# Kernel tuning notes

Hardware: AMD Instinct MI355X
Metric: run time of the kernel (lower is better)

## Reference

```python
import jax, jax.numpy as jnp
import numpy as np

N = 8192
F_IN = 256
F_OUT = 128
NEG_BIG = -9.0e15


def setup_inputs() -> dict:
    key = jax.random.key(0)
    k1, k2, k3, k4 = jax.random.split(key, 4)
    x = jax.random.normal(k1, (N, F_IN), dtype=jnp.float32)
    W = jax.random.normal(k2, (F_IN, F_OUT), dtype=jnp.float32) * 0.05
    a = jax.random.normal(k3, (2 * F_OUT, 1), dtype=jnp.float32) * 0.05
    adj = jax.random.randint(k4, (N, N), 0, 2, dtype=jnp.int32)
    return {"x": x, "W": W, "a": a, "adj": adj}


def reference(x, W, a, adj):
    # h = x @ W : [N, F_OUT]
    h = x @ W
    # Original builds [N, N, 2F] concat then matmuls with a. Since
    # a_input[i,j] = concat(h_i, h_j), the score is separable:
    # (a_input @ a)[i,j] = h_i . a[:F] + h_j . a[F:]
    a1 = a[:F_OUT, 0]   # [F_OUT]
    a2 = a[F_OUT:, 0]   # [F_OUT]
    s1 = h @ a1         # [N]
    s2 = h @ a2         # [N]
    e = jax.nn.leaky_relu(s1[:, None] + s2[None, :], negative_slope=0.2)
    e = jnp.where(adj > 0, e, jnp.float32(NEG_BIG))
    attention = jax.nn.softmax(e, axis=1)   # [N, N]
    h_prime = attention @ h                 # [N, F_OUT]
    return jax.nn.elu(h_prime)
```

## Files before the change

kernel.cpp:

```cpp
#include <hip/hip_runtime.h>
#include <math.h>

#define NN 8192

typedef __attribute__((ext_vector_type(8))) short short8;
typedef __attribute__((ext_vector_type(4))) short short4v;
typedef __attribute__((ext_vector_type(4))) float f32x4;
typedef __attribute__((ext_vector_type(4))) int int4v;

#define L2E 1.4426950408889634f

typedef __attribute__((address_space(3))) unsigned lds_u32;
typedef __attribute__((address_space(1))) unsigned g_u32;

__device__ __forceinline__ void gll16(const void* g, void* l) {
    __builtin_amdgcn_global_load_lds((const g_u32*)g, (lds_u32*)l, 16, 0, 0);
}

__device__ __forceinline__ short f2bf(float f) {
    union { float f; unsigned u; } v; v.f = f;
    unsigned r = v.u + 0x7fffu + ((v.u >> 16) & 1u);
    return (short)(r >> 16);
}

__device__ __forceinline__ f32x4 zero4() {
    f32x4 v; v[0] = 0.f; v[1] = 0.f; v[2] = 0.f; v[3] = 0.f; return v;
}

__global__ void k0_wt(const float* __restrict__ W, short* __restrict__ WT) {
    int idx = blockIdx.x * 256 + threadIdx.x;
    if (idx < 256 * 128) {
        int k = idx & 255;
        int f = idx >> 8;
        WT[f * 256 + k] = f2bf(W[k * 128 + f]);
    }
}

__global__ __launch_bounds__(128) void k1_h(
        const float* __restrict__ x, const short* __restrict__ WT,
        const float* __restrict__ a, short* __restrict__ hT,
        float* __restrict__ s1L2E, float* __restrict__ s2L2E) {
    const int w = threadIdx.x >> 6;
    const int l = threadIdx.x & 63;
    const int quad = l >> 4;
    const int fr = l & 15;
    const int i0 = blockIdx.x * 32 + w * 16;

    f32x4 acc[8];
#pragma unroll
    for (int t = 0; t < 8; ++t) acc[t] = zero4();

    const float* xrow = x + (size_t)(i0 + fr) * 256;
#pragma unroll
    for (int kk = 0; kk < 8; ++kk) {
        const int k0 = kk * 32 + quad * 8;
        f32x4 xa = *(const f32x4*)(xrow + k0);
        f32x4 xb = *(const f32x4*)(xrow + k0 + 4);
        short8 av;
#pragma unroll
        for (int e = 0; e < 4; ++e) { av[e] = f2bf(xa[e]); av[4 + e] = f2bf(xb[e]); }
#pragma unroll
        for (int t = 0; t < 8; ++t) {
            short8 bv = *(const short8*)(WT + (t * 16 + fr) * 256 + k0);
            acc[t] = __builtin_amdgcn_mfma_f32_16x16x32_bf16(av, bv, acc[t], 0, 0, 0);
        }
    }

    float s1p[4] = {0.f, 0.f, 0.f, 0.f};
    float s2p[4] = {0.f, 0.f, 0.f, 0.f};
#pragma unroll
    for (int t = 0; t < 8; ++t) {
        float a1v = a[t * 16 + fr];
        float a2v = a[128 + t * 16 + fr];
#pragma unroll
        for (int r = 0; r < 4; ++r) {
            s1p[r] += acc[t][r] * a1v;
            s2p[r] += acc[t][r] * a2v;
        }
    }
#pragma unroll
    for (int r = 0; r < 4; ++r) {
#pragma unroll
        for (int m = 1; m < 16; m <<= 1) {
            s1p[r] += __shfl_xor(s1p[r], m, 64);
            s2p[r] += __shfl_xor(s2p[r], m, 64);
        }
    }
    if (fr == 0) {
#pragma unroll
        for (int r = 0; r < 4; ++r) {
            const int i = i0 + quad * 4 + r;
            s1L2E[i] = s1p[r] * L2E;
            s2L2E[i] = s2p[r] * L2E;
        }
    }

#pragma unroll
    for (int t = 0; t < 8; ++t) {
        short4v hv;
#pragma unroll
        for (int r = 0; r < 4; ++r) hv[r] = f2bf(acc[t][r]);
        *(short4v*)(hT + (size_t)(t * 16 + fr) * NN + i0 + quad * 4) = hv;
    }
}

template<int JSPLIT, bool PARTIAL>
__global__ __launch_bounds__(256, 2) void k2_attn(
        const int* __restrict__ adj, const short* __restrict__ hT,
        const float* __restrict__ s1g, const float* __restrict__ s2g,
        float* __restrict__ pvp, float* __restrict__ zp,
        float* __restrict__ out) {
    constexpr int JW = NN / JSPLIT;
    constexpr int NSTEP = JW / 64;
    constexpr int BUFB = 25600;
    __shared__ __align__(16) char lds_c[3 * BUFB + 256];

    const int tid = threadIdx.x;
    const int w = tid >> 6;
    const int l = tid & 63;
    const int quad = l >> 4;
    const int fr = l & 15;
    const int rh = w >> 1;
    const int wj = w & 1;
    const int rb = blockIdx.x / JSPLIT;
    const int jb = blockIdx.x % JSPLIT;
    const int r32 = rb * 32;
    const int jbb = jb * JW;

    const float S = s1g[r32 + rh * 16 + fr];

    const char* hsrc[4];
    {
        const char* hbase = (const char*)hT;
#pragma unroll
        for (int p = 0; p < 4; ++p) {
            const int o = p * 4096 + tid * 16;
            const int row = o >> 7;
            const int colb = o & 127;
            hsrc[p] = hbase + (size_t)row * (NN * 2) + (size_t)jbb * 2
                    + (colb ^ ((row & 7) << 4));
        }
    }
    const char* asrc[2];
    {
        const char* abase = (const char*)adj;
#pragma unroll
        for (int p = 0; p < 2; ++p) {
            const int o = p * 4096 + tid * 16;
            const int row = o >> 8;
            const int colb = o & 255;
            asrc[p] = abase + (size_t)(r32 + row) * (NN * 4) + (size_t)jbb * 4
                    + (colb ^ ((row & 7) << 4));
        }
    }
    const char* csrc = (const char*)s2g + (size_t)jbb * 4 + (l < 16 ? l * 16 : 240);

    auto STAGE = [&](int jt, int buf) {
        jt = (jt < NSTEP) ? jt : NSTEP - 1;
        char* hd = lds_c + buf * BUFB + w * 1024;
        char* ad = lds_c + buf * BUFB + 16384 + w * 1024;
        char* cd = lds_c + buf * BUFB + 24576;
        const size_t hof = (size_t)jt * 128;
        const size_t aof = (size_t)jt * 256;
#pragma unroll
        for (int p = 0; p < 4; ++p) gll16(hsrc[p] + hof, hd + p * 4096);
#pragma unroll
        for (int p = 0; p < 2; ++p) gll16(asrc[p] + aof, ad + p * 4096);
        gll16(csrc + aof, cd);
    };

    f32x4 acc[8];
#pragma unroll
    for (int t = 0; t < 8; ++t) acc[t] = zero4();
    float zacc = 0.f;

    STAGE(0, 0); STAGE(1, 1); STAGE(2, 2);

    int cur = 0;
    for (int t = 0; t < NSTEP; ++t) {
        asm volatile("s_waitcnt vmcnt(14)" ::: "memory");
        __builtin_amdgcn_s_barrier();
        __builtin_amdgcn_sched_barrier(0);

        const char* hb = lds_c + cur * BUFB;
        const char* ab = lds_c + cur * BUFB + 16384;
        const float* cb = (const float*)(lds_c + cur * BUFB + 24576);

        const int arow = rh * 16 + fr;
        const unsigned aswz = (unsigned)((arow & 7) << 4);
        const unsigned al = (unsigned)(arow * 256 + wj * 128 + quad * 32);
        const int4v g0 = *(const int4v*)(ab + (al ^ aswz));
        const int4v g1 = *(const int4v*)(ab + ((al + 16) ^ aswz));
        const f32x4 c0 = *(const f32x4*)(cb + wj * 32 + quad * 8);
        const f32x4 c1 = *(const f32x4*)(cb + wj * 32 + quad * 8 + 4);

        short8 pa;
        {
            float zs = 0.f;
#pragma unroll
            for (int e = 0; e < 8; ++e) {
                const float cv = (e < 4) ? c0[e & 3] : c1[e & 3];
                const int gv = (e < 4) ? g0[e & 3] : g1[e & 3];
                const float u = S + cv;
                const float tt = fmaxf(u, 0.2f * u);
                const float p = (gv > 0) ? exp2f(tt) : 0.f;
                zs += p;
                pa[e] = f2bf(p);
            }
            zacc += zs;
        }

#pragma unroll
        for (int t8 = 0; t8 < 8; ++t8) {
            const int hrow = t8 * 16 + fr;
            const short8 bv = *(const short8*)(
                hb + ((unsigned)(hrow * 128 + wj * 64 + quad * 16) ^ ((hrow & 7) << 4)));
            acc[t8] = __builtin_amdgcn_mfma_f32_16x16x32_bf16(pa, bv, acc[t8], 0, 0, 0);
        }

        __builtin_amdgcn_sched_barrier(0);
        asm volatile("" ::: "memory");
        __builtin_amdgcn_s_barrier();

        STAGE(t + 3, cur);
        cur = (cur == 2) ? 0 : cur + 1;
    }

    asm volatile("s_waitcnt vmcnt(0)" ::: "memory");
    __syncthreads();

    zacc += __shfl_xor(zacc, 16, 64);
    zacc += __shfl_xor(zacc, 32, 64);
    float* zb = (float*)(lds_c + 3 * BUFB);
    if (l < 16) zb[w * 16 + l] = zacc;

    float* red = (float*)lds_c;
    if (wj == 1) {
#pragma unroll
        for (int t = 0; t < 8; ++t)
            *(f32x4*)(red + rh * 2048 + t * 256 + l * 4) = acc[t];
    }
    __syncthreads();

    if (wj == 0) {
#pragma unroll
        for (int t = 0; t < 8; ++t)
            acc[t] += *(const f32x4*)(red + rh * 2048 + t * 256 + l * 4);
#pragma unroll
        for (int r = 0; r < 4; ++r) {
            const int irow = quad * 4 + r;
            const float z = zb[rh * 32 + irow] + zb[rh * 32 + 16 + irow];
            const int grow = r32 + rh * 16 + irow;
            if (PARTIAL) {
                if (fr == 0) zp[(size_t)jb * NN + grow] = z;
                float* orow = pvp + ((size_t)jb * NN + grow) * 128;
#pragma unroll
                for (int t = 0; t < 8; ++t) orow[t * 16 + fr] = acc[t][r];
            } else {
                const float inv = 1.0f / z;
                float* orow = out + (size_t)grow * 128;
#pragma unroll
                for (int t = 0; t < 8; ++t) {
                    float v = acc[t][r] * inv;
                    orow[t * 16 + fr] = (v > 0.f) ? v : expm1f(v);
                }
            }
        }
    }
}

__global__ __launch_bounds__(256) void k3_fin(
        const float* __restrict__ pvp, const float* __restrict__ zp,
        float* __restrict__ out, int jsplit) {
    const int idx = blockIdx.x * 256 + threadIdx.x;
    const int row = idx >> 5;
    const int c = (idx & 31) << 2;
    f32x4 s = zero4();
    float z = 0.f;
    for (int p = 0; p < jsplit; ++p) {
        s += *(const f32x4*)(pvp + ((size_t)p * NN + row) * 128 + c);
        z += zp[(size_t)p * NN + row];
    }
    const float inv = 1.0f / z;
    f32x4 o;
#pragma unroll
    for (int e = 0; e < 4; ++e) {
        float v = s[e] * inv;
        o[e] = (v > 0.f) ? v : expm1f(v);
    }
    *(f32x4*)(out + (size_t)row * 128 + c) = o;
}

extern "C" void kernel_launch(void* const* d_in, const int* in_sizes, int n_in,
                              void* d_out, int out_size, void* d_ws, size_t ws_size,
                              hipStream_t stream) {
    const float* x   = (const float*)d_in[0];
    const float* W   = (const float*)d_in[1];
    const float* a   = (const float*)d_in[2];
    const int*   adj = (const int*)d_in[3];
    float* out = (float*)d_out;

    char* ws = (char*)d_ws;
    const size_t MB = 1024 * 1024;
    short* hT    = (short*)ws;
    float* s1L2E = (float*)(ws + 2 * MB);
    float* s2L2E = (float*)(ws + 2 * MB + 32768);
    short* WT    = (short*)(ws + 2 * MB + 65536);
    const size_t base = 2 * MB + 131072;

    const size_t need2 = base + 2 * ((size_t)NN * 128 * 4) + 2 * ((size_t)NN * 4);
    const bool js2 = (ws_size >= need2);

    float* pvp = (float*)(ws + base);
    float* zp  = (float*)(ws + base + (size_t)2 * NN * 128 * 4);

    k0_wt<<<128, 256, 0, stream>>>(W, WT);
    k1_h<<<256, 128, 0, stream>>>(x, WT, a, hT, s1L2E, s2L2E);

    if (js2) {
        k2_attn<2, true><<<512, 256, 0, stream>>>(adj, hT, s1L2E, s2L2E, pvp, zp, nullptr);
        k3_fin<<<1024, 256, 0, stream>>>(pvp, zp, out, 2);
    } else {
        k2_attn<1, false><<<256, 256, 0, stream>>>(adj, hT, s1L2E, s2L2E, nullptr, nullptr, out);
    }
}
```

Measured before the change: 94.73 us.

## Replace J-split attention with single-pass kernel using wide adj macro-tiles

Removes the two-way column split and the separate finalize kernel, so each 32-row block now streams all 8192 columns and writes the normalized ELU output directly. Adjacency is staged in 256-column macro tiles of contiguous 1KB row segments, double-buffered, while hT is quad-buffered in 64-column substeps. This is meant to cut partial-sum traffic and the extra launch, and to improve adj load granularity. In exchange it uses about 130KB of LDS, which forces one block per CU and halves resident waves, leaving less latency hiding.

Result: slower. 116.0 us (+22.5%).

```diff
diff --git a/kernel.cpp b/kernel.cpp
--- a/kernel.cpp
+++ b/kernel.cpp
@@ -104,16 +104,13 @@
     }
 }
 
-template<int JSPLIT, bool PARTIAL>
-__global__ __launch_bounds__(256, 2) void k2_attn(
+__global__ __launch_bounds__(256, 1) void k2_attn(
         const int* __restrict__ adj, const short* __restrict__ hT,
         const float* __restrict__ s1g, const float* __restrict__ s2g,
-        float* __restrict__ pvp, float* __restrict__ zp,
         float* __restrict__ out) {
-    constexpr int JW = NN / JSPLIT;
-    constexpr int NSTEP = JW / 64;
-    constexpr int BUFB = 25600;
-    __shared__ __align__(16) char lds_c[3 * BUFB + 256];
+    constexpr int NSUB = NN / 64;
+    constexpr int NMAC = NN / 256;
+    __shared__ __align__(16) char lds_c[133376];
 
     const int tid = threadIdx.x;
     const int w = tid >> 6;
@@ -122,10 +119,7 @@
     const int fr = l & 15;
     const int rh = w >> 1;
     const int wj = w & 1;
-    const int rb = blockIdx.x / JSPLIT;
-    const int jb = blockIdx.x % JSPLIT;
-    const int r32 = rb * 32;
-    const int jbb = jb * JW;
+    const int r32 = blockIdx.x * 32;
 
     const float S = s1g[r32 + rh * 16 + fr];
 
@@ -137,36 +131,32 @@
             const int o = p * 4096 + tid * 16;
             const int row = o >> 7;
             const int colb = o & 127;
-            hsrc[p] = hbase + (size_t)row * (NN * 2) + (size_t)jbb * 2
-                    + (colb ^ ((row & 7) << 4));
-        }
-    }
-    const char* asrc[2];
+            hsrc[p] = hbase + (size_t)row * (NN * 2) + (colb ^ ((row & 7) << 4));
+        }
+    }
+    const char* asrc8[8];
     {
         const char* abase = (const char*)adj;
 #pragma unroll
-        for (int p = 0; p < 2; ++p) {
-            const int o = p * 4096 + tid * 16;
-            const int row = o >> 8;
-            const int colb = o & 255;
-            asrc[p] = abase + (size_t)(r32 + row) * (NN * 4) + (size_t)jbb * 4
-                    + (colb ^ ((row & 7) << 4));
-        }
-    }
-    const char* csrc = (const char*)s2g + (size_t)jbb * 4 + (l < 16 ? l * 16 : 240);
-
-    auto STAGE = [&](int jt, int buf) {
-        jt = (jt < NSTEP) ? jt : NSTEP - 1;
-        char* hd = lds_c + buf * BUFB + w * 1024;
-        char* ad = lds_c + buf * BUFB + 16384 + w * 1024;
-        char* cd = lds_c + buf * BUFB + 24576;
-        const size_t hof = (size_t)jt * 128;
-        const size_t aof = (size_t)jt * 256;
+        for (int p = 0; p < 8; ++p) {
+            const int row = w * 8 + p;
+            asrc8[p] = abase + (size_t)(r32 + row) * (NN * 4) + ((l ^ p) << 4);
+        }
+    }
+    const char* csrc = (const char*)s2g + l * 16;
+
+    auto STAGE_HT = [&](int q, int buf) {
+        char* hd = lds_c + buf * 16384 + w * 1024;
+        const size_t hof = (size_t)q * 128;
 #pragma unroll
         for (int p = 0; p < 4; ++p) gll16(hsrc[p] + hof, hd + p * 4096);
-#pragma unroll
-        for (int p = 0; p < 2; ++p) gll16(asrc[p] + aof, ad + p * 4096);
-        gll16(csrc + aof, cd);
+    };
+    auto STAGE_AC = [&](int m, int buf) {
+        char* ad = lds_c + 65536 + buf * 32768 + w * 8192;
+        const size_t aof = (size_t)m * 1024;
+#pragma unroll
+        for (int p = 0; p < 8; ++p) gll16(asrc8[p] + aof, ad + p * 1024);
+        gll16(csrc + aof, lds_c + 131072 + buf * 1024);
     };
 
     f32x4 acc[8];
@@ -174,41 +164,34 @@
     for (int t = 0; t < 8; ++t) acc[t] = zero4();
     float zacc = 0.f;
 
-    STAGE(0, 0); STAGE(1, 1); STAGE(2, 2);
-
-    int cur = 0;
-    for (int t = 0; t < NSTEP; ++t) {
-        asm volatile("s_waitcnt vmcnt(14)" ::: "memory");
-        __builtin_amdgcn_s_barrier();
-        __builtin_amdgcn_sched_barrier(0);
-
-        const char* hb = lds_c + cur * BUFB;
-        const char* ab = lds_c + cur * BUFB + 16384;
-        const float* cb = (const float*)(lds_c + cur * BUFB + 24576);
-
-        const int arow = rh * 16 + fr;
-        const unsigned aswz = (unsigned)((arow & 7) << 4);
-        const unsigned al = (unsigned)(arow * 256 + wj * 128 + quad * 32);
-        const int4v g0 = *(const int4v*)(ab + (al ^ aswz));
-        const int4v g1 = *(const int4v*)(ab + ((al + 16) ^ aswz));
-        const f32x4 c0 = *(const f32x4*)(cb + wj * 32 + quad * 8);
-        const f32x4 c1 = *(const f32x4*)(cb + wj * 32 + quad * 8 + 4);
+    const int arow = rh * 16 + fr;
+    const unsigned r7 = (unsigned)(arow & 7);
+
+    auto COMPUTE = [&](int q) {
+        const char* hb = lds_c + (q & 3) * 16384;
+        const char* ab = lds_c + 65536 + ((q >> 2) & 1) * 32768;
+        const float* cb = (const float*)(lds_c + 131072 + ((q >> 2) & 1) * 1024);
+        const int sl = q & 3;
+
+        const unsigned cch = (unsigned)(sl * 16 + wj * 8 + quad * 2);
+        const int4v g0 = *(const int4v*)(ab + arow * 1024 + ((cch ^ r7) << 4));
+        const int4v g1 = *(const int4v*)(ab + arow * 1024 + (((cch + 1) ^ r7) << 4));
+        const f32x4 c0 = *(const f32x4*)(cb + sl * 64 + wj * 32 + quad * 8);
+        const f32x4 c1 = *(const f32x4*)(cb + sl * 64 + wj * 32 + quad * 8 + 4);
 
         short8 pa;
-        {
-            float zs = 0.f;
-#pragma unroll
-            for (int e = 0; e < 8; ++e) {
-                const float cv = (e < 4) ? c0[e & 3] : c1[e & 3];
-                const int gv = (e < 4) ? g0[e & 3] : g1[e & 3];
-                const float u = S + cv;
-                const float tt = fmaxf(u, 0.2f * u);
-                const float p = (gv > 0) ? exp2f(tt) : 0.f;
-                zs += p;
-                pa[e] = f2bf(p);
-            }
-            zacc += zs;
-        }
+        float zs = 0.f;
+#pragma unroll
+        for (int e = 0; e < 8; ++e) {
+            const float cv = (e < 4) ? c0[e & 3] : c1[e & 3];
+            const int gv = (e < 4) ? g0[e & 3] : g1[e & 3];
+            const float u = S + cv;
+            const float tt = fmaxf(u, 0.2f * u);
+            const float p = (gv > 0) ? exp2f(tt) : 0.f;
+            zs += p;
+            pa[e] = f2bf(p);
+        }
+        zacc += zs;
 
 #pragma unroll
         for (int t8 = 0; t8 < 8; ++t8) {
@@ -217,21 +200,45 @@
                 hb + ((unsigned)(hrow * 128 + wj * 64 + quad * 16) ^ ((hrow & 7) << 4)));
             acc[t8] = __builtin_amdgcn_mfma_f32_16x16x32_bf16(pa, bv, acc[t8], 0, 0, 0);
         }
-
-        __builtin_amdgcn_sched_barrier(0);
-        asm volatile("" ::: "memory");
-        __builtin_amdgcn_s_barrier();
-
-        STAGE(t + 3, cur);
-        cur = (cur == 2) ? 0 : cur + 1;
-    }
+    };
+
+    STAGE_AC(0, 0);
+    STAGE_HT(0, 0); STAGE_HT(1, 1); STAGE_HT(2, 2); STAGE_HT(3, 3);
+
+#define SUBSTEP(S_, VMLIT)                                            \
+    {                                                                 \
+        asm volatile("s_waitcnt vmcnt(" #VMLIT ")" ::: "memory");     \
+        __builtin_amdgcn_s_barrier();                                 \
+        __builtin_amdgcn_sched_barrier(0);                            \
+        COMPUTE(m * 4 + S_);                                          \
+        __builtin_amdgcn_sched_barrier(0);                            \
+        asm volatile("" ::: "memory");                                \
+        __builtin_amdgcn_s_barrier();                                 \
+        if (S_ == 0) {                                                \
+            const int mm = (m + 1 < NMAC) ? m + 1 : NMAC - 1;         \
+            STAGE_AC(mm, (m + 1) & 1);                                \
+        }                                                             \
+        {                                                             \
+            int qq = m * 4 + S_ + 4;                                  \
+            if (qq > NSUB - 1) qq = NSUB - 1;                         \
+            STAGE_HT(qq, S_);                                         \
+        }                                                             \
+    }
+
+    for (int m = 0; m < NMAC; ++m) {
+        SUBSTEP(0, 12)
+        SUBSTEP(1, 21)
+        SUBSTEP(2, 21)
+        SUBSTEP(3, 21)
+    }
+#undef SUBSTEP
 
     asm volatile("s_waitcnt vmcnt(0)" ::: "memory");
     __syncthreads();
 
     zacc += __shfl_xor(zacc, 16, 64);
     zacc += __shfl_xor(zacc, 32, 64);
-    float* zb = (float*)(lds_c + 3 * BUFB);
+    float* zb = (float*)(lds_c + 133120);
     if (l < 16) zb[w * 16 + l] = zacc;
 
     float* red = (float*)lds_c;
@@ -251,44 +258,15 @@
             const int irow = quad * 4 + r;
             const float z = zb[rh * 32 + irow] + zb[rh * 32 + 16 + irow];
             const int grow = r32 + rh * 16 + irow;
-            if (PARTIAL) {
-                if (fr == 0) zp[(size_t)jb * NN + grow] = z;
-                float* orow = pvp + ((size_t)jb * NN + grow) * 128;
-#pragma unroll
-                for (int t = 0; t < 8; ++t) orow[t * 16 + fr] = acc[t][r];
-            } else {
-                const float inv = 1.0f / z;
-                float* orow = out + (size_t)grow * 128;
-#pragma unroll
-                for (int t = 0; t < 8; ++t) {
-                    float v = acc[t][r] * inv;
-                    orow[t * 16 + fr] = (v > 0.f) ? v : expm1f(v);
-                }
+            const float inv = 1.0f / z;
+            float* orow = out + (size_t)grow * 128;
+#pragma unroll
+            for (int t = 0; t < 8; ++t) {
+                float v = acc[t][r] * inv;
+                orow[t * 16 + fr] = (v > 0.f) ? v : expm1f(v);
             }
         }
     }
-}
-
-__global__ __launch_bounds__(256) void k3_fin(
-        const float* __restrict__ pvp, const float* __restrict__ zp,
-        float* __restrict__ out, int jsplit) {
-    const int idx = blockIdx.x * 256 + threadIdx.x;
-    const int row = idx >> 5;
-    const int c = (idx & 31) << 2;
-    f32x4 s = zero4();
-    float z = 0.f;
-    for (int p = 0; p < jsplit; ++p) {
-        s += *(const f32x4*)(pvp + ((size_t)p * NN + row) * 128 + c);
-        z += zp[(size_t)p * NN + row];
-    }
-    const float inv = 1.0f / z;
-    f32x4 o;
-#pragma unroll
-    for (int e = 0; e < 4; ++e) {
-        float v = s[e] * inv;
-        o[e] = (v > 0.f) ? v : expm1f(v);
-    }
-    *(f32x4*)(out + (size_t)row * 128 + c) = o;
 }
 
 extern "C" void kernel_launch(void* const* d_in, const int* in_sizes, int n_in,
@@ -306,21 +284,8 @@
     float* s1L2E = (float*)(ws + 2 * MB);
     float* s2L2E = (float*)(ws + 2 * MB + 32768);
     short* WT    = (short*)(ws + 2 * MB + 65536);
-    const size_t base = 2 * MB + 131072;
-
-    const size_t need2 = base + 2 * ((size_t)NN * 128 * 4) + 2 * ((size_t)NN * 4);
-    const bool js2 = (ws_size >= need2);
-
-    float* pvp = (float*)(ws + base);
-    float* zp  = (float*)(ws + base + (size_t)2 * NN * 128 * 4);
 
     k0_wt<<<128, 256, 0, stream>>>(W, WT);
     k1_h<<<256, 128, 0, stream>>>(x, WT, a, hT, s1L2E, s2L2E);
-
-    if (js2) {
-        k2_attn<2, true><<<512, 256, 0, stream>>>(adj, hT, s1L2E, s2L2E, pvp, zp, nullptr);
-        k3_fin<<<1024, 256, 0, stream>>>(pvp, zp, out, 2);
-    } else {
-        k2_attn<1, false><<<256, 256, 0, stream>>>(adj, hT, s1L2E, s2L2E, nullptr, nullptr, out);
-    }
-}
+    k2_attn<<<256, 256, 0, stream>>>(adj, hT, s1L2E, s2L2E, out);
+}
```
